# Optimization experiments

Measured on AMD Instinct MI355X. Metric: run time of the kernel, lower is better.

## Reference

```python
import jax, jax.numpy as jnp
import numpy as np

EPS_DISC = 1e-9  # matches mamba_discretization denominator epsilon


def setup_inputs() -> dict:
    key = jax.random.key(0)
    ks = jax.random.split(key, 12)
    L, D, N, W = 2048, 1024, 16, 3
    s = 0.02  # small init scale to keep softplus/exp well-behaved
    u_seq = jax.random.normal(ks[0], (L, D), jnp.float32)
    # A_log = log(-A) with A = randn*0.1 - 1.0  -> log of a value near 1
    A_log = jnp.log(jnp.clip(1.0 - 0.1 * jax.random.normal(ks[1], (N,), jnp.float32), 0.5, 1.5))
    dt_w = jax.random.normal(ks[2], (D, D), jnp.float32) * s
    dt_b = jax.random.normal(ks[3], (D,), jnp.float32) * s
    B_w = jax.random.normal(ks[4], (N, D), jnp.float32) * s
    B_b = jax.random.normal(ks[5], (N,), jnp.float32) * s
    C_w = jax.random.normal(ks[6], (N, D), jnp.float32) * s
    C_b = jax.random.normal(ks[7], (N,), jnp.float32) * s
    D_w = jnp.ones((D,), jnp.float32)
    scale = jnp.ones((), jnp.float32)
    init_w = jax.random.normal(ks[8], (D * N, D * W), jnp.float32) * s
    init_b = jax.random.normal(ks[9], (D * N,), jnp.float32) * s
    return {"u_seq": u_seq, "A_log": A_log, "dt_w": dt_w, "dt_b": dt_b,
            "B_w": B_w, "B_b": B_b, "C_w": C_w, "C_b": C_b,
            "D_w": D_w, "scale": scale, "init_w": init_w, "init_b": init_b}


def reference(u_seq, A_log, dt_w, dt_b, B_w, B_b, C_w, C_b, D_w, scale, init_w, init_b):
    L, D = u_seq.shape
    N = A_log.shape[0]
    init_window = init_w.shape[1] // D
    # Initial state h0 = init_estimator(u[:W].flatten()).view(D, N)
    u_prefix = u_seq[:init_window].reshape(-1)
    h0 = (u_prefix @ init_w.T + init_b).reshape(D, N)
    # Input-dependent SSM parameters (all L timesteps at once)
    dt = jax.nn.softplus(u_seq @ dt_w.T + dt_b)           # [L, D]
    B = u_seq @ B_w.T + B_b                               # [L, N]
    C = u_seq @ C_w.T + C_b                               # [L, N]
    A = -jnp.exp(A_log)                                   # [N]
    dtA = dt[:, :, None] * A                              # [L, D, N]
    dA = jnp.exp(dtA)                                     # [L, D, N]
    dB = jnp.expm1(dtA) / (dtA + EPS_DISC) * B[:, None, :]  # ZOH discretization
    Bu = dB * u_seq[:, :, None]                           # [L, D, N]

    # Sequential selective-scan recurrence: h_t = dA_t * h_{t-1} + Bu_t
    def step(h, inp):
        dA_t, Bu_t = inp
        h = dA_t * h + Bu_t
        return h, h

    _, h_hist = jax.lax.scan(step, h0, (dA, Bu))          # [L, D, N]
    y_raw = jnp.einsum('ln,ldn->ld', C, h_hist) + D_w * u_seq
    return jax.nn.softplus(y_raw) * jnp.maximum(scale, 0.5)
```

## Files before the change

kernel.cpp:

```cpp
#include <hip/hip_runtime.h>
#include <hip/hip_bf16.h>

typedef __attribute__((ext_vector_type(8))) short short8v;
typedef __attribute__((ext_vector_type(4))) float f32x4;

#define L_SEQ 2048
#define D_DIM 1024
#define N_DIM 16
#define T_CHUNK 32
#define NCHUNK (L_SEQ / T_CHUNK)
#define EPS_DISC 1e-9f

__device__ __forceinline__ float softplusf(float x) {
    return (x > 15.f) ? x : __logf(1.f + __expf(x));
}

__device__ __forceinline__ unsigned short f2bf(float f) {
    unsigned int u = __float_as_uint(f);
    u += 0x7FFFu + ((u >> 16) & 1u);
    return (unsigned short)(u >> 16);
}
__device__ __forceinline__ unsigned int pack2(float a, float b) {
    return (unsigned int)f2bf(a) | ((unsigned int)f2bf(b) << 16);
}
__device__ __forceinline__ float dot4(float4 a, float4 b) {
    return a.x * b.x + a.y * b.y + a.z * b.z + a.w * b.w;
}

__global__ __launch_bounds__(256, 4) void k_mv(const float* __restrict__ u,
                                               const float* __restrict__ init_w,
                                               const float* __restrict__ init_b,
                                               float* __restrict__ h0) {
    __shared__ float red[8];
    const int slab = blockIdx.x;
    const int t = threadIdx.x;
    const int wv = t >> 6, lane = t & 63;

    const float4* u4 = (const float4*)u;
    const float4 u0 = u4[t];
    const float4 u1 = u4[t + 256];
    const float4 u2 = u4[t + 512];

    const float4* w4 = (const float4*)init_w + (size_t)slab * 1536;
    const float4 w0 = w4[t];
    const float4 w1 = w4[t + 256];
    const float4 w2 = w4[t + 512];
    const float4 w3 = w4[t + 768];
    const float4 w4v = w4[t + 1024];
    const float4 w5 = w4[t + 1280];

    float acc0 = dot4(w0, u0) + dot4(w1, u1) + dot4(w2, u2);
    float acc1 = dot4(w3, u0) + dot4(w4v, u1) + dot4(w5, u2);

#pragma unroll
    for (int m = 32; m >= 1; m >>= 1) {
        acc0 += __shfl_down(acc0, m);
        acc1 += __shfl_down(acc1, m);
    }
    if (lane == 0) { red[wv] = acc0; red[wv + 4] = acc1; }
    __syncthreads();
    if (t < 2) {
        const float s = red[t * 4 + 0] + red[t * 4 + 1] + red[t * 4 + 2] + red[t * 4 + 3];
        const int row = slab * 2 + t;
        h0[row] = s + init_b[row];
    }
}

__global__ __launch_bounds__(256) void k_gemm_bc(const float* __restrict__ u,
                                                 const float* __restrict__ dt_w,
                                                 const float* __restrict__ dt_b,
                                                 const float* __restrict__ B_w,
                                                 const float* __restrict__ B_b,
                                                 const float* __restrict__ C_w,
                                                 const float* __restrict__ C_b,
                                                 float* __restrict__ dt,
                                                 float* __restrict__ Bm,
                                                 float* __restrict__ Cm) {
    __shared__ unsigned int smem[3072];
    const int b = blockIdx.x;
    const int t = threadIdx.x;

    if (b < 256) {
        unsigned int* As = smem;
        unsigned int* Bs = smem + 1024;
        const int bm = b & 31;
        const int bn = b >> 5;
        const int lane = t & 63;
        const int wn   = t >> 6;
        const int lrow = lane & 15, lq = lane >> 4;

        const int arow = t >> 2, aq = t & 3;
        const int brow = t >> 1, bhalf = t & 1;

        const float* uptr = u + (bm * 64 + arow) * 1024 + aq * 8;
        const float* wptr = dt_w + (bn * 128 + brow) * 1024 + bhalf * 16;

        f32x4 acc[4][2];
#pragma unroll
        for (int mi = 0; mi < 4; ++mi)
#pragma unroll
            for (int ni = 0; ni < 2; ++ni) acc[mi][ni] = (f32x4){0.f, 0.f, 0.f, 0.f};

        for (int k0 = 0; k0 < 1024; k0 += 32) {
            __syncthreads();
            {
                const float4* p = (const float4*)(uptr + k0);
                float4 a0 = p[0], a1 = p[1];
                uint4 ca = make_uint4(pack2(a0.x, a0.y), pack2(a0.z, a0.w),
                                      pack2(a1.x, a1.y), pack2(a1.z, a1.w));
                const int akb = aq ^ ((arow >> 1) & 3);
                *(uint4*)&As[arow * 16 + akb * 4] = ca;

                const float4* q = (const float4*)(wptr + k0);
                float4 b0 = q[0], b1 = q[1], b2 = q[2], b3 = q[3];
                uint4 d0 = make_uint4(pack2(b0.x, b0.y), pack2(b0.z, b0.w),
                                      pack2(b1.x, b1.y), pack2(b1.z, b1.w));
                uint4 d1 = make_uint4(pack2(b2.x, b2.y), pack2(b2.z, b2.w),
                                      pack2(b3.x, b3.y), pack2(b3.z, b3.w));
                const int bswz = (brow >> 1) & 3;
                const int kb0 = (bhalf * 2) ^ bswz, kb1 = (bhalf * 2 + 1) ^ bswz;
                *(uint4*)&Bs[brow * 16 + kb0 * 4] = d0;
                *(uint4*)&Bs[brow * 16 + kb1 * 4] = d1;
            }
            __syncthreads();
            short8v af[4], bf[2];
#pragma unroll
            for (int mi = 0; mi < 4; ++mi) {
                const int ar = mi * 16 + lrow;
                const int kb = lq ^ ((ar >> 1) & 3);
                af[mi] = *(const short8v*)&As[ar * 16 + kb * 4];
            }
#pragma unroll
            for (int ni = 0; ni < 2; ++ni) {
                const int br = wn * 32 + ni * 16 + lrow;
                const int kb = lq ^ ((br >> 1) & 3);
                bf[ni] = *(const short8v*)&Bs[br * 16 + kb * 4];
            }
#pragma unroll
            for (int mi = 0; mi < 4; ++mi)
#pragma unroll
                for (int ni = 0; ni < 2; ++ni)
                    acc[mi][ni] = __builtin_amdgcn_mfma_f32_16x16x32_bf16(af[mi], bf[ni], acc[mi][ni], 0, 0, 0);
        }

#pragma unroll
        for (int mi = 0; mi < 4; ++mi)
#pragma unroll
            for (int ni = 0; ni < 2; ++ni) {
                const int cg = bn * 128 + wn * 32 + ni * 16 + lrow;
                const float bv = dt_b[cg];
#pragma unroll
                for (int j = 0; j < 4; ++j) {
                    const int rg = bm * 64 + mi * 16 + lq * 4 + j;
                    dt[rg * 1024 + cg] = softplusf(acc[mi][ni][j] + bv);
                }
            }
    } else {
        const int s2 = b - 256;
        const int wv = t >> 6, lane = t & 63;
#pragma unroll
        for (int rep = 0; rep < 2; ++rep) {
            const int l = s2 * 8 + wv * 2 + rep;
            const float4* u4 = (const float4*)(u + l * 1024);
            float4 ur[4];
#pragma unroll
            for (int i = 0; i < 4; ++i) ur[i] = u4[i * 64 + lane];
#pragma unroll 4
            for (int c = 0; c < 32; ++c) {
                const float4* wr = (const float4*)((c < 16) ? (B_w + c * 1024)
                                                            : (C_w + (c - 16) * 1024));
                float sv = 0.f;
#pragma unroll
                for (int i = 0; i < 4; ++i) sv += dot4(ur[i], wr[i * 64 + lane]);
#pragma unroll
                for (int off = 32; off > 0; off >>= 1) sv += __shfl_down(sv, off);
                if (lane == 0) {
                    if (c < 16) Bm[l * 16 + c] = sv + B_b[c];
                    else        Cm[l * 16 + (c - 16)] = sv + C_b[c - 16];
                }
            }
        }
    }
}

__global__ __launch_bounds__(256) void k_p1(const float* __restrict__ dt,
                                            const float* __restrict__ Bm,
                                            const float* __restrict__ u,
                                            const float* __restrict__ A_log,
                                            float* __restrict__ ap,
                                            float* __restrict__ hl) {
    const int t    = threadIdx.x;
    const int c    = blockIdx.x >> 3;
    const int dblk = blockIdx.x & 7;
    const int dd   = t >> 1;
    const int nh   = t & 1;
    const int d    = dblk * 128 + dd;
    float An[8];
#pragma unroll
    for (int n = 0; n < 8; ++n) An[n] = -__expf(A_log[nh * 8 + n]);
    float h[8], p[8];
#pragma unroll
    for (int n = 0; n < 8; ++n) { h[n] = 0.f; p[n] = 1.f; }

    const int l0 = c * T_CHUNK;
    for (int i = 0; i < T_CHUNK; ++i) {
        const int l = l0 + i;
        const float dtld = dt[l * D_DIM + d];
        const float uld  = u[l * D_DIM + d];
        const float4 b0 = *(const float4*)&Bm[l * 16 + nh * 8];
        const float4 b1 = *(const float4*)&Bm[l * 16 + nh * 8 + 4];
        auto body = [&](int n, float bn) {
            const float x = dtld * An[n];
            const float e = __expf(x);
            const float coef = (e - 1.f) * __builtin_amdgcn_rcpf(x + EPS_DISC);
            const float bu = coef * bn * uld;
            p[n] *= e;
            h[n] = fmaf(e, h[n], bu);
        };
        body(0, b0.x); body(1, b0.y); body(2, b0.z); body(3, b0.w);
        body(4, b1.x); body(5, b1.y); body(6, b1.z); body(7, b1.w);
    }
    const int base = c * (D_DIM * N_DIM) + d * 16 + nh * 8;
    *(float4*)&ap[base + 0] = make_float4(p[0], p[1], p[2], p[3]);
    *(float4*)&ap[base + 4] = make_float4(p[4], p[5], p[6], p[7]);
    *(float4*)&hl[base + 0] = make_float4(h[0], h[1], h[2], h[3]);
    *(float4*)&hl[base + 4] = make_float4(h[4], h[5], h[6], h[7]);
}

__global__ __launch_bounds__(64) void k_p2(const float* __restrict__ h0,
                                           float* __restrict__ ap,
                                           const float* __restrict__ hl) {
    const int ch = blockIdx.x * 64 + threadIdx.x;
    float h = h0[ch];
#pragma unroll 8
    for (int c = 0; c < NCHUNK; ++c) {
        const int idx = c * (D_DIM * N_DIM) + ch;
        const float a = ap[idx];
        const float b = hl[idx];
        ap[idx] = h;
        h = fmaf(a, h, b);
    }
}

__global__ __launch_bounds__(256) void k_p3(const float* __restrict__ dt,
                                            const float* __restrict__ Bm,
                                            const float* __restrict__ Cm,
                                            const float* __restrict__ u,
                                            const float* __restrict__ A_log,
                                            const float* __restrict__ hstart,
                                            const float* __restrict__ D_w,
                                            const float* __restrict__ scale,
                                            float* __restrict__ out) {
    const int t    = threadIdx.x;
    const int c    = blockIdx.x >> 3;
    const int dblk = blockIdx.x & 7;
    const int dd   = t >> 1;
    const int nh   = t & 1;
    const int d    = dblk * 128 + dd;
    float An[8];
#pragma unroll
    for (int n = 0; n < 8; ++n) An[n] = -__expf(A_log[nh * 8 + n]);
    float h[8];
    const int base = c * (D_DIM * N_DIM) + d * 16 + nh * 8;
    {
        float4 h0v = *(const float4*)&hstart[base + 0];
        float4 h1v = *(const float4*)&hstart[base + 4];
        h[0] = h0v.x; h[1] = h0v.y; h[2] = h0v.z; h[3] = h0v.w;
        h[4] = h1v.x; h[5] = h1v.y; h[6] = h1v.z; h[7] = h1v.w;
    }
    const float scl = fmaxf(scale[0], 0.5f);
    const float dw = D_w[d];
    const int l0 = c * T_CHUNK;
    for (int i = 0; i < T_CHUNK; ++i) {
        const int l = l0 + i;
        const float dtld = dt[l * D_DIM + d];
        const float uld  = u[l * D_DIM + d];
        const float4 b0 = *(const float4*)&Bm[l * 16 + nh * 8];
        const float4 b1 = *(const float4*)&Bm[l * 16 + nh * 8 + 4];
        const float4 c0 = *(const float4*)&Cm[l * 16 + nh * 8];
        const float4 c1 = *(const float4*)&Cm[l * 16 + nh * 8 + 4];
        float y = 0.f;
        auto body = [&](int n, float bn, float cn) {
            const float x = dtld * An[n];
            const float e = __expf(x);
            const float coef = (e - 1.f) * __builtin_amdgcn_rcpf(x + EPS_DISC);
            const float bu = coef * bn * uld;
            h[n] = fmaf(e, h[n], bu);
            y = fmaf(cn, h[n], y);
        };
        body(0, b0.x, c0.x); body(1, b0.y, c0.y); body(2, b0.z, c0.z); body(3, b0.w, c0.w);
        body(4, b1.x, c1.x); body(5, b1.y, c1.y); body(6, b1.z, c1.z); body(7, b1.w, c1.w);
        y += __shfl_xor(y, 1);
        if (nh == 0) {
            const float yv = fmaf(dw, uld, y);
            out[l * D_DIM + d] = softplusf(yv) * scl;
        }
    }
}

extern "C" void kernel_launch(void* const* d_in, const int* in_sizes, int n_in,
                              void* d_out, int out_size, void* d_ws, size_t ws_size,
                              hipStream_t stream) {
    const float* u      = (const float*)d_in[0];
    const float* A_log  = (const float*)d_in[1];
    const float* dt_w   = (const float*)d_in[2];
    const float* dt_b   = (const float*)d_in[3];
    const float* B_w    = (const float*)d_in[4];
    const float* B_b    = (const float*)d_in[5];
    const float* C_w    = (const float*)d_in[6];
    const float* C_b    = (const float*)d_in[7];
    const float* D_w    = (const float*)d_in[8];
    const float* scale  = (const float*)d_in[9];
    const float* init_w = (const float*)d_in[10];
    const float* init_b = (const float*)d_in[11];
    float* out = (float*)d_out;

    float* ws = (float*)d_ws;
    float* dt = ws;
    float* Bm = dt + 2097152;
    float* Cm = Bm + 32768;
    float* h0 = Cm + 32768;
    float* ap = h0 + 16384;
    float* hl = ap + 1048576;

    hipLaunchKernelGGL(k_mv,      dim3(8192), dim3(256), 0, stream, u, init_w, init_b, h0);
    hipLaunchKernelGGL(k_gemm_bc, dim3(512),  dim3(256), 0, stream,
                       u, dt_w, dt_b, B_w, B_b, C_w, C_b, dt, Bm, Cm);
    hipLaunchKernelGGL(k_p1, dim3(512), dim3(256), 0, stream, dt, Bm, u, A_log, ap, hl);
    hipLaunchKernelGGL(k_p2, dim3(256), dim3(64), 0, stream, h0, ap, hl);
    hipLaunchKernelGGL(k_p3, dim3(512), dim3(256), 0, stream, dt, Bm, Cm, u, A_log, ap, D_w, scale, out);
}
```

Baseline: 127.2 us.

## Split init-state matvec across GEMM and chunk-scan kernels to overlap work

The standalone h0 matvec kernel, which streams the large init_w matrix, is removed. Its 8192 slabs are split between the GEMM/BC kernel (extra blocks after index 512) and the chunk-scan phase-1 kernel (remaining slabs). The bandwidth-bound matvec can then run alongside the compute-bound MFMA GEMM and the latency-bound scan, and one launch is saved. The split point is a hand-tuned constant, and the extra blocks in k_d1 share that kernel's larger smem allocation and launch bounds, which may reduce occupancy.

```diff
diff --git a/kernel.cpp b/kernel.cpp
--- a/kernel.cpp
+++ b/kernel.cpp
@@ -10,6 +10,7 @@
 #define T_CHUNK 32
 #define NCHUNK (L_SEQ / T_CHUNK)
 #define EPS_DISC 1e-9f
+#define MV_SPLIT 4915
 
 __device__ __forceinline__ float softplusf(float x) {
     return (x > 15.f) ? x : __logf(1.f + __expf(x));
@@ -27,15 +28,13 @@
     return a.x * b.x + a.y * b.y + a.z * b.z + a.w * b.w;
 }
 
-__global__ __launch_bounds__(256, 4) void k_mv(const float* __restrict__ u,
-                                               const float* __restrict__ init_w,
-                                               const float* __restrict__ init_b,
-                                               float* __restrict__ h0) {
-    __shared__ float red[8];
-    const int slab = blockIdx.x;
-    const int t = threadIdx.x;
+__device__ __forceinline__ void mv_slab(int slab, int t,
+                                        const float* __restrict__ u,
+                                        const float* __restrict__ init_w,
+                                        const float* __restrict__ init_b,
+                                        float* __restrict__ h0,
+                                        float* red ) {
     const int wv = t >> 6, lane = t & 63;
-
     const float4* u4 = (const float4*)u;
     const float4 u0 = u4[t];
     const float4 u1 = u4[t + 256];
@@ -66,16 +65,19 @@
     }
 }
 
-__global__ __launch_bounds__(256) void k_gemm_bc(const float* __restrict__ u,
-                                                 const float* __restrict__ dt_w,
-                                                 const float* __restrict__ dt_b,
-                                                 const float* __restrict__ B_w,
-                                                 const float* __restrict__ B_b,
-                                                 const float* __restrict__ C_w,
-                                                 const float* __restrict__ C_b,
-                                                 float* __restrict__ dt,
-                                                 float* __restrict__ Bm,
-                                                 float* __restrict__ Cm) {
+__global__ __launch_bounds__(256) void k_d1(const float* __restrict__ u,
+                                            const float* __restrict__ dt_w,
+                                            const float* __restrict__ dt_b,
+                                            const float* __restrict__ B_w,
+                                            const float* __restrict__ B_b,
+                                            const float* __restrict__ C_w,
+                                            const float* __restrict__ C_b,
+                                            const float* __restrict__ init_w,
+                                            const float* __restrict__ init_b,
+                                            float* __restrict__ dt,
+                                            float* __restrict__ Bm,
+                                            float* __restrict__ Cm,
+                                            float* __restrict__ h0) {
     __shared__ unsigned int smem[3072];
     const int b = blockIdx.x;
     const int t = threadIdx.x;
@@ -155,7 +157,7 @@
                     dt[rg * 1024 + cg] = softplusf(acc[mi][ni][j] + bv);
                 }
             }
-    } else {
+    } else if (b < 512) {
         const int s2 = b - 256;
         const int wv = t >> 6, lane = t & 63;
 #pragma unroll
@@ -180,18 +182,31 @@
                 }
             }
         }
-    }
-}
-
-__global__ __launch_bounds__(256) void k_p1(const float* __restrict__ dt,
+    } else {
+        mv_slab(b - 512, t, u, init_w, init_b, h0, (float*)smem);
+    }
+}
+
+__global__ __launch_bounds__(256) void k_d2(const float* __restrict__ dt,
                                             const float* __restrict__ Bm,
                                             const float* __restrict__ u,
                                             const float* __restrict__ A_log,
+                                            const float* __restrict__ init_w,
+                                            const float* __restrict__ init_b,
                                             float* __restrict__ ap,
-                                            float* __restrict__ hl) {
-    const int t    = threadIdx.x;
-    const int c    = blockIdx.x >> 3;
-    const int dblk = blockIdx.x & 7;
+                                            float* __restrict__ hl,
+                                            float* __restrict__ h0) {
+    __shared__ float red[8];
+    const int b = blockIdx.x;
+    const int t = threadIdx.x;
+
+    if (b >= 512) {
+        mv_slab(MV_SPLIT + (b - 512), t, u, init_w, init_b, h0, red);
+        return;
+    }
+
+    const int c    = b >> 3;
+    const int dblk = b & 7;
     const int dd   = t >> 1;
     const int nh   = t & 1;
     const int d    = dblk * 128 + dd;
@@ -323,10 +338,11 @@
     float* ap = h0 + 16384;
     float* hl = ap + 1048576;
 
-    hipLaunchKernelGGL(k_mv,      dim3(8192), dim3(256), 0, stream, u, init_w, init_b, h0);
-    hipLaunchKernelGGL(k_gemm_bc, dim3(512),  dim3(256), 0, stream,
-                       u, dt_w, dt_b, B_w, B_b, C_w, C_b, dt, Bm, Cm);
-    hipLaunchKernelGGL(k_p1, dim3(512), dim3(256), 0, stream, dt, Bm, u, A_log, ap, hl);
+    hipLaunchKernelGGL(k_d1, dim3(512 + MV_SPLIT), dim3(256), 0, stream,
+                       u, dt_w, dt_b, B_w, B_b, C_w, C_b, init_w, init_b,
+                       dt, Bm, Cm, h0);
+    hipLaunchKernelGGL(k_d2, dim3(512 + (8192 - MV_SPLIT)), dim3(256), 0, stream,
+                       dt, Bm, u, A_log, init_w, init_b, ap, hl, h0);
     hipLaunchKernelGGL(k_p2, dim3(256), dim3(64), 0, stream, h0, ap, hl);
     hipLaunchKernelGGL(k_p3, dim3(512), dim3(256), 0, stream, dt, Bm, Cm, u, A_log, ap, D_w, scale, out);
 }
```

After: 115.0 us. -9.6%, faster.
